# Optimization experiments

Hardware: AMD Instinct MI355X
Metric: run time of the kernel (lower is better)

## Reference

```python
import jax, jax.numpy as jnp
import numpy as np

OUT, IN, GROUP = 8192, 8192, 128  # meta.shape=(out,in), group_size over out dim


def unpack_int4(packed, out_shape):
    """Unpack uint8 bytes (two nibbles each) into signed int8 in [-8,7].
    Matches torch: inter[0::2]=lo, inter[1::2]=hi."""
    flat = packed.reshape(-1)
    lo = (flat & 15).astype(jnp.int8)
    hi = ((flat >> 4) & 15).astype(jnp.int8)
    lo = jnp.where(lo >= 8, lo - 16, lo)
    hi = jnp.where(hi >= 8, hi - 16, hi)
    inter = jnp.stack([lo, hi], axis=-1).reshape(-1)  # interleave lo/hi
    total = out_shape[0] * out_shape[1]
    return inter[:total].reshape(out_shape)


def setup_inputs() -> dict:
    key = jax.random.key(0)
    kx, kq, ks, kb = jax.random.split(key, 4)
    x = jax.random.normal(kx, (16, IN), dtype=jnp.float32)
    # packed int4 weights: one byte holds two nibbles -> OUT*IN/2 bytes
    q_packed = jax.random.randint(kq, (OUT * IN // 2,), 0, 256, dtype=jnp.int32).astype(jnp.uint8)
    # per-group scales (group over out dim), positive small values
    scale = jax.random.uniform(ks, (OUT // GROUP,), dtype=jnp.float32) * 0.01 + 1e-4
    bias = jax.random.normal(kb, (OUT,), dtype=jnp.float32) * 0.01
    return {"x": x, "q_packed": q_packed, "scale": scale, "bias": bias}


def reference(x, q_packed, scale, bias):
    # unpack + per-group dequant, then matmul (CPU fallback path of QuantLinear.forward)
    q_int = unpack_int4(q_packed, (OUT, IN)).astype(jnp.float32)  # (OUT, IN)
    s = jnp.repeat(scale, GROUP)[:, None]                         # (OUT, 1) expanded scales
    W = s * q_int                                                 # dequantized fp weight
    return x @ W.T + bias                                         # (B, OUT)
```

## Files before the change

kernel.cpp:

```cpp
#include <hip/hip_runtime.h>
#include <hip/hip_bf16.h>

#define OUT_N 8192
#define IN_N  8192
#define QROW  (IN_N / 2)
#define NCH   8
#define CH32  64

typedef __attribute__((ext_vector_type(8))) short short8v;
typedef __attribute__((ext_vector_type(4))) float f32x4;

__device__ __forceinline__ unsigned int bf16pk(float a, float b) {
    __hip_bfloat162 h = __float22bfloat162_rn(make_float2(a, b));
    unsigned int u;
    __builtin_memcpy(&u, &h, 4);
    return u;
}

#define SCHED0() __builtin_amdgcn_sched_barrier(0)
#define WAITV(n) asm volatile("s_waitcnt vmcnt(" #n ")" ::: "memory")
#define WAITL()  asm volatile("s_waitcnt lgkmcnt(0)" ::: "memory")

__global__ __launch_bounds__(256) void xconv_kernel(
    const float* __restrict__ x, uint4* __restrict__ xb2)
{
    const int tid = blockIdx.x * 256 + threadIdx.x;
    const int l   = tid & 63;
    const int scs = tid >> 6;
    const int s   = scs & 3;
    const int c   = (scs >> 2) & 7;
    const int w   = scs >> 5;
    const int r   = l & 15;
    const int g   = l >> 4;
    const float* src = x + (size_t)r * IN_N + w * 1024 + c * 128 + s * 32 + g * 8;
    float4 a = *(const float4*)src;
    float4 b = *(const float4*)(src + 4);
    uint4 u = { bf16pk(a.x, a.y), bf16pk(a.z, a.w),
                bf16pk(b.x, b.y), bf16pk(b.z, b.w) };
    xb2[tid] = u;
}

__global__ __launch_bounds__(512, 4) void qlin_mfma_kernel(
    const int*   __restrict__ qp,
    const uint4* __restrict__ xb2,
    const float* __restrict__ scale,
    const float* __restrict__ bias,
    float*       __restrict__ out)
{
    __shared__ int   qbuf[8][2][16 * CH32];
    __shared__ float red[8][16][17];

    const int t = threadIdx.x;
    const int w = t >> 6;
    const int l = t & 63;
    const int g = l >> 4;
    const int r = l & 15;
    const int tile = blockIdx.x;
    const int obase = tile * 16;
    const int ph = tile & 7;

    const int* qwbase = qp + (size_t)obase * QROW + w * (QROW / 8);
    const int drow = l >> 4;
    const uint4* xwbase = xb2 + (w << 11) + l;

    f32x4 acc = {0.f, 0.f, 0.f, 0.f};
    int4  qr0, qr1, qr2, qr3;
    uint4 xa0, xa1, xa2, xa3;
    uint4 xb0, xb1, xb2r, xb3;

#define QLD(c_) do {                                                          \
    const int cc = ((c_) + ph) & 7;                                           \
    const int r0 = 0 + drow, r1 = 4 + drow, r2 = 8 + drow, r3 = 12 + drow;    \
    qr0 = *(const int4*)(qwbase + (size_t)r0 * QROW + cc * CH32 + (((l & 15) ^ r0) << 2)); \
    qr1 = *(const int4*)(qwbase + (size_t)r1 * QROW + cc * CH32 + (((l & 15) ^ r1) << 2)); \
    qr2 = *(const int4*)(qwbase + (size_t)r2 * QROW + cc * CH32 + (((l & 15) ^ r2) << 2)); \
    qr3 = *(const int4*)(qwbase + (size_t)r3 * QROW + cc * CH32 + (((l & 15) ^ r3) << 2)); \
    } while (0)

#define XLD(c_, B0, B1, B2, B3) do {                                          \
    const int cc = ((c_) + ph) & 7;                                           \
    B0 = xwbase[cc * 256 +   0]; B1 = xwbase[cc * 256 +  64];                 \
    B2 = xwbase[cc * 256 + 128]; B3 = xwbase[cc * 256 + 192];                 \
    } while (0)

#define QST(PAR) do {                                                         \
    *(int4*)&qbuf[w][PAR][0 * 256 + l * 4] = qr0;                             \
    *(int4*)&qbuf[w][PAR][1 * 256 + l * 4] = qr1;                             \
    *(int4*)&qbuf[w][PAR][2 * 256 + l * 4] = qr2;                             \
    *(int4*)&qbuf[w][PAR][3 * 256 + l * 4] = qr3;                             \
    } while (0)

#define STEP(PAR, S, XV) do {                                                 \
    const int4 q = *(const int4*)((const char*)qbuf[w][PAR] + r * 256         \
                                  + (((((S) << 2) + g) ^ r) << 4));           \
    uint4 ub = {                                                              \
        bf16pk((float)((q.x << 28) >> 28), (float)((q.x << 24) >> 28)),       \
        bf16pk((float)((q.y << 28) >> 28), (float)((q.y << 24) >> 28)),       \
        bf16pk((float)((q.z << 28) >> 28), (float)((q.z << 24) >> 28)),       \
        bf16pk((float)((q.w << 28) >> 28), (float)((q.w << 24) >> 28))        \
    };                                                                        \
    short8v bfrag = __builtin_bit_cast(short8v, ub);                          \
    short8v afrag = __builtin_bit_cast(short8v, XV);                          \
    acc = __builtin_amdgcn_mfma_f32_16x16x32_bf16(afrag, bfrag, acc, 0, 0, 0);\
    } while (0)

#define COMPUTE(PAR, B0, B1, B2, B3) do {                                     \
    STEP(PAR, 0, B0); STEP(PAR, 1, B1); STEP(PAR, 2, B2); STEP(PAR, 3, B3);   \
    } while (0)

#define BODY(PAR, NPAR, CB0, CB1, CB2, CB3, NB0, NB1, NB2, NB3, Cp2)          \
    do {                                                                      \
        WAITL(); SCHED0();                                                    \
        COMPUTE(PAR, CB0, CB1, CB2, CB3);                                     \
        SCHED0(); WAITV(4); SCHED0();                \
        QST(NPAR);                                                            \
        QLD(Cp2); XLD(Cp2, CB0, CB1, CB2, CB3);      \
        SCHED0(); WAITV(8); SCHED0();                    \
    } while (0)

    QLD(0); XLD(0, xa0, xa1, xa2, xa3);
    WAITV(4); SCHED0();
    QST(0);
    QLD(1); XLD(1, xb0, xb1, xb2r, xb3);
    WAITV(8); SCHED0();

    BODY(0, 1, xa0, xa1, xa2, xa3, xb0, xb1, xb2r, xb3, 2);
    BODY(1, 0, xb0, xb1, xb2r, xb3, xa0, xa1, xa2, xa3, 3);
    BODY(0, 1, xa0, xa1, xa2, xa3, xb0, xb1, xb2r, xb3, 4);
    BODY(1, 0, xb0, xb1, xb2r, xb3, xa0, xa1, xa2, xa3, 5);
    BODY(0, 1, xa0, xa1, xa2, xa3, xb0, xb1, xb2r, xb3, 6);
    BODY(1, 0, xb0, xb1, xb2r, xb3, xa0, xa1, xa2, xa3, 7);
    WAITL(); SCHED0();
    COMPUTE(0, xa0, xa1, xa2, xa3);
    SCHED0(); WAITV(4); SCHED0();
    QST(1);
    WAITV(0); SCHED0();
    WAITL(); SCHED0();
    COMPUTE(1, xb0, xb1, xb2r, xb3);

#undef QLD
#undef XLD
#undef QST
#undef STEP
#undef COMPUTE
#undef BODY

    red[w][g * 4 + 0][r] = acc[0];
    red[w][g * 4 + 1][r] = acc[1];
    red[w][g * 4 + 2][r] = acc[2];
    red[w][g * 4 + 3][r] = acc[3];
    __syncthreads();

    if (t < 256) {
        const int b = t >> 4;
        const int o = t & 15;
        const int oc = obase + o;
        float v = 0.f;
        #pragma unroll
        for (int i = 0; i < 8; ++i) v += red[i][b][o];
        out[b * OUT_N + oc] = v * scale[oc >> 7] + bias[oc];
    }
}

extern "C" void kernel_launch(void* const* d_in, const int* in_sizes, int n_in,
                              void* d_out, int out_size, void* d_ws, size_t ws_size,
                              hipStream_t stream) {
    (void)in_sizes; (void)n_in; (void)ws_size; (void)out_size;
    const float* x     = (const float*)d_in[0];
    const int*   qp    = (const int*)d_in[1];
    const float* scale = (const float*)d_in[2];
    const float* bias  = (const float*)d_in[3];
    float*       out   = (float*)d_out;
    uint4*       xb2   = (uint4*)d_ws;

    xconv_kernel<<<dim3(64), dim3(256), 0, stream>>>(x, xb2);
    qlin_mfma_kernel<<<dim3(OUT_N / 16), dim3(512), 0, stream>>>(qp, xb2, scale, bias, out);
}
```

Before: 30.28 us.

## Fuse fp32-to-bf16 activation conversion into the GEMV kernel, drop pre-pass launch

Removes the separate xconv kernel that converted x to a bf16 fragment layout in workspace. The main kernel now loads fp32 x directly with float4 loads, converts to bf16 in registers, and re-times the vmcnt waits and prefetch pipeline to fit. This saves a kernel launch and a workspace round trip. In exchange each of the 512 blocks converts x redundantly, reads twice the activation bytes, and uses more VGPRs for eight float4 staging registers.

Measured after the change: 39.33 us. 29.9% more time.

```diff
diff --git a/kernel.cpp b/kernel.cpp
--- a/kernel.cpp
+++ b/kernel.cpp
@@ -4,7 +4,6 @@
 #define OUT_N 8192
 #define IN_N  8192
 #define QROW  (IN_N / 2)
-#define NCH   8
 #define CH32  64
 
 typedef __attribute__((ext_vector_type(8))) short short8v;
@@ -21,28 +20,9 @@
 #define WAITV(n) asm volatile("s_waitcnt vmcnt(" #n ")" ::: "memory")
 #define WAITL()  asm volatile("s_waitcnt lgkmcnt(0)" ::: "memory")
 
-__global__ __launch_bounds__(256) void xconv_kernel(
-    const float* __restrict__ x, uint4* __restrict__ xb2)
-{
-    const int tid = blockIdx.x * 256 + threadIdx.x;
-    const int l   = tid & 63;
-    const int scs = tid >> 6;
-    const int s   = scs & 3;
-    const int c   = (scs >> 2) & 7;
-    const int w   = scs >> 5;
-    const int r   = l & 15;
-    const int g   = l >> 4;
-    const float* src = x + (size_t)r * IN_N + w * 1024 + c * 128 + s * 32 + g * 8;
-    float4 a = *(const float4*)src;
-    float4 b = *(const float4*)(src + 4);
-    uint4 u = { bf16pk(a.x, a.y), bf16pk(a.z, a.w),
-                bf16pk(b.x, b.y), bf16pk(b.z, b.w) };
-    xb2[tid] = u;
-}
-
 __global__ __launch_bounds__(512, 4) void qlin_mfma_kernel(
     const int*   __restrict__ qp,
-    const uint4* __restrict__ xb2,
+    const float* __restrict__ x,
     const float* __restrict__ scale,
     const float* __restrict__ bias,
     float*       __restrict__ out)
@@ -61,12 +41,12 @@
 
     const int* qwbase = qp + (size_t)obase * QROW + w * (QROW / 8);
     const int drow = l >> 4;
-    const uint4* xwbase = xb2 + (w << 11) + l;
+    const float* xwbase = x + (size_t)r * IN_N + w * (IN_N / 8) + g * 8;
 
     f32x4 acc = {0.f, 0.f, 0.f, 0.f};
-    int4  qr0, qr1, qr2, qr3;
-    uint4 xa0, xa1, xa2, xa3;
-    uint4 xb0, xb1, xb2r, xb3;
+    int4   qr0, qr1, qr2, qr3;
+    float4 xf0, xf1, xf2, xf3, xf4, xf5, xf6, xf7;
+    uint4  xc0, xc1, xc2, xc3;
 
 #define QLD(c_) do {                                                          \
     const int cc = ((c_) + ph) & 7;                                           \
@@ -77,10 +57,24 @@
     qr3 = *(const int4*)(qwbase + (size_t)r3 * QROW + cc * CH32 + (((l & 15) ^ r3) << 2)); \
     } while (0)
 
-#define XLD(c_, B0, B1, B2, B3) do {                                          \
+#define XFLD(c_) do {                                                         \
     const int cc = ((c_) + ph) & 7;                                           \
-    B0 = xwbase[cc * 256 +   0]; B1 = xwbase[cc * 256 +  64];                 \
-    B2 = xwbase[cc * 256 + 128]; B3 = xwbase[cc * 256 + 192];                 \
+    const float* xp = xwbase + cc * 128;                                      \
+    xf0 = *(const float4*)(xp +   0); xf1 = *(const float4*)(xp +   4);       \
+    xf2 = *(const float4*)(xp +  32); xf3 = *(const float4*)(xp +  36);       \
+    xf4 = *(const float4*)(xp +  64); xf5 = *(const float4*)(xp +  68);       \
+    xf6 = *(const float4*)(xp +  96); xf7 = *(const float4*)(xp + 100);       \
+    } while (0)
+
+#define CONVERT() do {                                                        \
+    xc0 = (uint4){ bf16pk(xf0.x, xf0.y), bf16pk(xf0.z, xf0.w),                \
+                   bf16pk(xf1.x, xf1.y), bf16pk(xf1.z, xf1.w) };              \
+    xc1 = (uint4){ bf16pk(xf2.x, xf2.y), bf16pk(xf2.z, xf2.w),                \
+                   bf16pk(xf3.x, xf3.y), bf16pk(xf3.z, xf3.w) };              \
+    xc2 = (uint4){ bf16pk(xf4.x, xf4.y), bf16pk(xf4.z, xf4.w),                \
+                   bf16pk(xf5.x, xf5.y), bf16pk(xf5.z, xf5.w) };              \
+    xc3 = (uint4){ bf16pk(xf6.x, xf6.y), bf16pk(xf6.z, xf6.w),                \
+                   bf16pk(xf7.x, xf7.y), bf16pk(xf7.z, xf7.w) };              \
     } while (0)
 
 #define QST(PAR) do {                                                         \
@@ -104,42 +98,47 @@
     acc = __builtin_amdgcn_mfma_f32_16x16x32_bf16(afrag, bfrag, acc, 0, 0, 0);\
     } while (0)
 
-#define COMPUTE(PAR, B0, B1, B2, B3) do {                                     \
-    STEP(PAR, 0, B0); STEP(PAR, 1, B1); STEP(PAR, 2, B2); STEP(PAR, 3, B3);   \
+#define COMPUTE(PAR) do {                                                     \
+    STEP(PAR, 0, xc0); STEP(PAR, 1, xc1); STEP(PAR, 2, xc2); STEP(PAR, 3, xc3); \
     } while (0)
 
-#define BODY(PAR, NPAR, CB0, CB1, CB2, CB3, NB0, NB1, NB2, NB3, Cp2)          \
-    do {                                                                      \
+#define BODY(PAR, NPAR, Cp2) do {                                             \
         WAITL(); SCHED0();                                                    \
-        COMPUTE(PAR, CB0, CB1, CB2, CB3);                                     \
-        SCHED0(); WAITV(4); SCHED0();                \
+        COMPUTE(PAR);                                                         \
+        SCHED0(); WAITV(8); SCHED0();                     \
         QST(NPAR);                                                            \
-        QLD(Cp2); XLD(Cp2, CB0, CB1, CB2, CB3);      \
-        SCHED0(); WAITV(8); SCHED0();                    \
+        QLD(Cp2);                                     \
+        SCHED0(); WAITV(4); SCHED0();                    \
+        CONVERT();                                           \
+        XFLD(Cp2);                                    \
     } while (0)
 
-    QLD(0); XLD(0, xa0, xa1, xa2, xa3);
+    QLD(0); XFLD(0);
+    WAITV(8); SCHED0();
+    QST(0);
+    QLD(1);
     WAITV(4); SCHED0();
-    QST(0);
-    QLD(1); XLD(1, xb0, xb1, xb2r, xb3);
-    WAITV(8); SCHED0();
+    CONVERT();
+    XFLD(1);
 
-    BODY(0, 1, xa0, xa1, xa2, xa3, xb0, xb1, xb2r, xb3, 2);
-    BODY(1, 0, xb0, xb1, xb2r, xb3, xa0, xa1, xa2, xa3, 3);
-    BODY(0, 1, xa0, xa1, xa2, xa3, xb0, xb1, xb2r, xb3, 4);
-    BODY(1, 0, xb0, xb1, xb2r, xb3, xa0, xa1, xa2, xa3, 5);
-    BODY(0, 1, xa0, xa1, xa2, xa3, xb0, xb1, xb2r, xb3, 6);
-    BODY(1, 0, xb0, xb1, xb2r, xb3, xa0, xa1, xa2, xa3, 7);
+    BODY(0, 1, 2);
+    BODY(1, 0, 3);
+    BODY(0, 1, 4);
+    BODY(1, 0, 5);
+    BODY(0, 1, 6);
+    BODY(1, 0, 7);
     WAITL(); SCHED0();
-    COMPUTE(0, xa0, xa1, xa2, xa3);
-    SCHED0(); WAITV(4); SCHED0();
+    COMPUTE(0);
+    SCHED0(); WAITV(8); SCHED0();
     QST(1);
     WAITV(0); SCHED0();
+    CONVERT();
     WAITL(); SCHED0();
-    COMPUTE(1, xb0, xb1, xb2r, xb3);
+    COMPUTE(1);
 
 #undef QLD
-#undef XLD
+#undef XFLD
+#undef CONVERT
 #undef QST
 #undef STEP
 #undef COMPUTE
@@ -165,14 +164,12 @@
 extern "C" void kernel_launch(void* const* d_in, const int* in_sizes, int n_in,
                               void* d_out, int out_size, void* d_ws, size_t ws_size,
                               hipStream_t stream) {
-    (void)in_sizes; (void)n_in; (void)ws_size; (void)out_size;
+    (void)in_sizes; (void)n_in; (void)d_ws; (void)ws_size; (void)out_size;
     const float* x     = (const float*)d_in[0];
     const int*   qp    = (const int*)d_in[1];
     const float* scale = (const float*)d_in[2];
     const float* bias  = (const float*)d_in[3];
     float*       out   = (float*)d_out;
-    uint4*       xb2   = (uint4*)d_ws;
 
-    xconv_kernel<<<dim3(64), dim3(256), 0, stream>>>(x, xb2);
-    qlin_mfma_kernel<<<dim3(OUT_N / 16), dim3(512), 0, stream>>>(qp, xb2, scale, bias, out);
+    qlin_mfma_kernel<<<dim3(OUT_N / 16), dim3(512), 0, stream>>>(qp, x, scale, bias, out);
 }
```
